# Kernel optimization log

Measured on AMD Instinct MI355X. Metric: run time of the kernel, lower is better.

## Reference

```python
import jax, jax.numpy as jnp
import numpy as np
import math

B, T, D_MODEL, N_HEADS = 4, 2048, 1024, 16
HEAD_DIM = D_MODEL // N_HEADS


def setup_inputs() -> dict:
    key = jax.random.key(0)
    k1, k2, k3 = jax.random.split(key, 3)
    x = jax.random.normal(k1, (B, T, D_MODEL), dtype=jnp.float32)
    # torch Linear weight layout: [out_features, in_features]
    w_qkv = jax.random.normal(k2, (3 * D_MODEL, D_MODEL), dtype=jnp.float32) * (1.0 / math.sqrt(D_MODEL))
    w_out = jax.random.normal(k3, (D_MODEL, D_MODEL), dtype=jnp.float32) * (1.0 / math.sqrt(D_MODEL))
    return {"x": x, "w_qkv": w_qkv, "w_out": w_out}


def reference(x, w_qkv, w_out):
    b, t, c = x.shape
    h, d = N_HEADS, HEAD_DIM
    # qkv projection: (B,T,3C) -> (3,B,H,T,D)
    qkv = jnp.einsum('btc,fc->btf', x, w_qkv)
    qkv = qkv.reshape(b, t, 3, h, d).transpose(2, 0, 3, 1, 4)
    q, k, v = qkv[0], qkv[1], qkv[2]
    scale = 1.0 / math.sqrt(d)
    # full O(T^2) attention scores, causal masked
    scores = jnp.einsum('bhqd,bhkd->bhqk', q, k) * scale
    causal = jnp.tril(jnp.ones((t, t), dtype=bool))
    scores = jnp.where(causal[None, None, :, :], scores, jnp.float32(-jnp.inf))
    attn = jax.nn.softmax(scores, axis=-1)
    out = jnp.einsum('bhqk,bhkd->bhqd', attn, v)  # (B,H,T,D)
    out = out.transpose(0, 2, 1, 3).reshape(b, t, c)
    out = jnp.einsum('btc,oc->bto', out, w_out)
    return out
```

## Files before the change

### kernel.cpp

```cpp
#include <hip/hip_runtime.h>
#include <hip/hip_bf16.h>

#define T_SEQ 2048
#define BATCH 4
#define NH    16
#define DM    1024
#define HD    64

typedef __attribute__((ext_vector_type(4))) float  f32x4;
typedef __attribute__((ext_vector_type(8))) short  s16x8;
typedef __attribute__((ext_vector_type(4))) short  s16x4;

__device__ __forceinline__ unsigned short f2b(float f) {
  union { float f; unsigned u; } v; v.f = f;
  unsigned u = v.u;
  unsigned r = 0x7fffu + ((u >> 16) & 1u);
  u += r;
  return (unsigned short)(u >> 16);
}

__device__ __forceinline__ f32x4 mfma16(s16x8 a, s16x8 b, f32x4 c) {
  return __builtin_amdgcn_mfma_f32_16x16x32_bf16(a, b, c, 0, 0, 0);
}

__device__ __forceinline__ float exp2_fast(float x) {
  float r; asm("v_exp_f32 %0, %1" : "=v"(r) : "v"(x)); return r;
}

__device__ __forceinline__ unsigned cvt_pk_bf16(float lo, float hi) {
  unsigned r; asm("v_cvt_pk_bf16_f32 %0, %1, %2" : "=v"(r) : "v"(lo), "v"(hi)); return r;
}

#define BAR() __builtin_amdgcn_s_barrier()
#define SCB() __builtin_amdgcn_sched_barrier(0)
#define LGK(n) do { asm volatile("s_waitcnt lgkmcnt(" #n ")" ::: "memory"); SCB(); } while (0)
#define VMC(n) do { asm volatile("s_waitcnt vmcnt(" #n ")" ::: "memory"); } while (0)

__global__ void cvt_all(const float* __restrict__ x, const float* __restrict__ wq,
                        const float* __restrict__ wo,
                        unsigned short* __restrict__ xb, unsigned short* __restrict__ wqb,
                        unsigned short* __restrict__ wob) {
  const int N4X = (BATCH * T_SEQ * DM) / 4;
  const int N4Q = (3 * DM * DM) / 4;
  const int N4O = (DM * DM) / 4;
  const int N4QSCALED = (DM * DM) / 4;
  int i = blockIdx.x * blockDim.x + threadIdx.x;
  int stride = gridDim.x * blockDim.x;
  for (int j = i; j < N4X + N4Q + N4O; j += stride) {
    const float* src; unsigned short* dst; int k; float scale = 1.f;
    if (j < N4X) { src = x; dst = xb; k = j; }
    else if (j < N4X + N4Q) {
      k = j - N4X; src = wq; dst = wqb;
      if (k < N4QSCALED) scale = 0.18033688011112042f;
    } else { k = j - N4X - N4Q; src = wo; dst = wob; }
    f32x4 v = ((const f32x4*)src)[k];
    s16x4 o;
    o.x = (short)f2b(v.x * scale); o.y = (short)f2b(v.y * scale);
    o.z = (short)f2b(v.z * scale); o.w = (short)f2b(v.w * scale);
    ((s16x4*)dst)[k] = o;
  }
}

__device__ __forceinline__ void rd4(s16x8 (&d)[4], const char* base, int rbase, int cb) {
#pragma unroll
  for (int j = 0; j < 4; ++j)
    d[j] = *(const s16x8*)(base + (rbase + j * 16) * 128 + cb);
}

__device__ __forceinline__ void stage_half(const unsigned short* __restrict__ Msrc,
                                           int rt0, int kt, char* lbase, int half,
                                           int srow8, int c2src, int c2lin, int Kd) {
#pragma unroll
  for (int q = 0; q < 2; ++q) {
    int rl = half * 128 + q * 64 + srow8;
    const char* src = (const char*)(Msrc + (size_t)(rt0 + rl) * Kd + kt) + c2src;
    __builtin_amdgcn_global_load_lds((const void*)src, (void*)(lbase + rl * 128 + c2lin),
                                     16, 0, 0);
  }
}

__device__ __forceinline__ void clust(f32x4 (&acc)[8][4], const s16x8 (&a)[4],
                                      const s16x8 (&b)[4], int mb) {
  __builtin_amdgcn_s_setprio(1);
#pragma unroll
  for (int j = 0; j < 4; ++j)
#pragma unroll
    for (int n = 0; n < 4; ++n)
      acc[mb + j][n] = mfma16(a[j], b[n], acc[mb + j][n]);
  __builtin_amdgcn_s_setprio(0);
}

__global__ __launch_bounds__(512, 2)
void gemm8p(const unsigned short* __restrict__ A, const unsigned short* __restrict__ B,
            unsigned short* __restrict__ C, int M, int N, int K) {
  __shared__ char smem[131072];
  char* A0b = smem;
  char* A1b = smem + 32768;
  char* B0b = smem + 65536;
  char* B1b = smem + 98304;

  const int tid = threadIdx.x;
  const int lane = tid & 63;
  const int w = tid >> 6;
  const int wm = w >> 2, wn = w & 3;
  const int lr = lane & 15, g = lane >> 4;

  const int gx = gridDim.x, nwg = gx * gridDim.y;
  const int bid = blockIdx.y * gx + blockIdx.x;
  const int cpx = nwg >> 3;
  const int b2 = (bid & 7) * cpx + (bid >> 3);
  const int row0 = (b2 % gx) * 256;
  const int col0 = (b2 / gx) * 256;

  const int srow8 = tid >> 3;
  const int c2lin = (tid & 7) * 16;
  const int c2src = ((tid & 7) ^ (srow8 & 7)) * 16;

  const int swz = (lr & 7) << 4;
  const int cs0 = (g * 16) ^ swz;
  const int cs1 = (64 + g * 16) ^ swz;
  const int rAlo = wm * 128 + lr;
  const int rAhi = rAlo + 64;
  const int rB = wn * 64 + lr;

  f32x4 acc[8][4] = {};
  s16x8 aP[4], aQ[4], aR[4], bP[4], bQ[4];

  const int NT = K / 64;

  stage_half(A, row0, 0, A0b, 0, srow8, c2src, c2lin, K);
  stage_half(A, row0, 0, A0b, 1, srow8, c2src, c2lin, K);
  stage_half(B, col0, 0, B0b, 0, srow8, c2src, c2lin, K);
  stage_half(B, col0, 0, B0b, 1, srow8, c2src, c2lin, K);
  stage_half(A, row0, 64, A1b, 0, srow8, c2src, c2lin, K);
  VMC(2);
  BAR();
  rd4(aP, A0b, rAlo, cs0);
  rd4(bP, B0b, rB, cs0);

  auto body = [&](char* Ac, char* Bc, char* An, char* Bn, int t) {
    const int ktn  = min(t + 1, NT - 1) * 64;
    const int ktn2 = min(t + 2, NT - 1) * 64;
    rd4(aQ, Ac, rAhi, cs0);
    stage_half(A, row0, ktn, An, 1, srow8, c2src, c2lin, K);
    BAR(); LGK(4);
    clust(acc, aP, bP, 0);
    BAR();
    rd4(aP, Ac, rAlo, cs1);
    rd4(aR, Ac, rAhi, cs1);
    rd4(bQ, Bc, rB, cs1);
    stage_half(B, col0, ktn, Bn, 0, srow8, c2src, c2lin, K);
    BAR(); LGK(12);
    clust(acc, aQ, bP, 4);
    BAR();
    stage_half(B, col0, ktn, Bn, 1, srow8, c2src, c2lin, K);
    BAR(); LGK(0);
    clust(acc, aP, bQ, 0);
    BAR();
    stage_half(A, row0, ktn2, Ac, 0, srow8, c2src, c2lin, K);
    VMC(2);
    BAR();
    rd4(aP, An, rAlo, cs0);
    rd4(bP, Bn, rB, cs0);
    clust(acc, aR, bQ, 4);
    BAR();
  };

#pragma unroll 1
  for (int tt = 0; tt < NT; tt += 2) {
    body(A0b, B0b, A1b, B1b, tt);
    body(A1b, B1b, A0b, B0b, tt + 1);
  }

#pragma unroll
  for (int m = 0; m < 8; ++m)
#pragma unroll
    for (int n = 0; n < 4; ++n)
#pragma unroll
      for (int i = 0; i < 4; ++i) {
        int row = row0 + wm * 128 + m * 16 + g * 4 + i;
        int col = col0 + wn * 64 + n * 16 + lr;
        C[(size_t)row * N + col] = f2b(acc[m][n][i]);
      }
}

template<int OUT_F32>
__global__ __launch_bounds__(256)
void gemm_bt(const unsigned short* __restrict__ A,
             const unsigned short* __restrict__ B,
             void* __restrict__ C, int M, int N, int K) {
  __shared__ unsigned short As[128 * 32];
  __shared__ unsigned short Bs[128 * 32];
  const int tid  = threadIdx.x;
  const int lane = tid & 63;
  const int w    = tid >> 6;
  const int wr   = w >> 1, wc = w & 1;
  const int lr   = lane & 15, g = lane >> 4;

  const int gx  = gridDim.x, nwg = gx * gridDim.y;
  const int bid = blockIdx.y * gx + blockIdx.x;
  const int cpx = nwg >> 3;
  const int b2  = (bid & 7) * cpx + (bid >> 3);
  const int row0 = (b2 % gx) * 128;
  const int col0 = (b2 / gx) * 128;

  const int srow = w * 16 + (lane >> 2);
  const int scol = (lane & 3) * 8;

  f32x4 acc[4][4] = {};

  for (int kt = 0; kt < K; kt += 32) {
    __syncthreads();
#pragma unroll
    for (int s = 0; s < 2; ++s) {
      const unsigned short* srcA = A + (size_t)(row0 + s * 64 + srow) * K + kt + scol;
      __builtin_amdgcn_global_load_lds((const void*)srcA, (void*)&As[(s * 64 + w * 16) * 32], 16, 0, 0);
      const unsigned short* srcB = B + (size_t)(col0 + s * 64 + srow) * K + kt + scol;
      __builtin_amdgcn_global_load_lds((const void*)srcB, (void*)&Bs[(s * 64 + w * 16) * 32], 16, 0, 0);
    }
    __syncthreads();

    s16x8 af[4], bf[4];
#pragma unroll
    for (int m = 0; m < 4; ++m)
      af[m] = *(const s16x8*)&As[(wr * 64 + m * 16 + lr) * 32 + g * 8];
#pragma unroll
    for (int n = 0; n < 4; ++n)
      bf[n] = *(const s16x8*)&Bs[(wc * 64 + n * 16 + lr) * 32 + g * 8];
#pragma unroll
    for (int m = 0; m < 4; ++m)
#pragma unroll
      for (int n = 0; n < 4; ++n)
        acc[m][n] = mfma16(af[m], bf[n], acc[m][n]);
  }

#pragma unroll
  for (int m = 0; m < 4; ++m)
#pragma unroll
    for (int n = 0; n < 4; ++n)
#pragma unroll
      for (int i = 0; i < 4; ++i) {
        int row = row0 + wr * 64 + m * 16 + g * 4 + i;
        int col = col0 + wc * 64 + n * 16 + lr;
        if (OUT_F32)
          ((float*)C)[(size_t)row * N + col] = acc[m][n][i];
        else
          ((unsigned short*)C)[(size_t)row * N + col] = f2b(acc[m][n][i]);
      }
}

__global__ __launch_bounds__(512)
void attn_kernel(const unsigned short* __restrict__ qkv,
                 unsigned short* __restrict__ out) {
  __shared__ unsigned short Ks[2][64 * 64];
  __shared__ unsigned short Vt[2][64 * 72];
  __shared__ unsigned short Ps[8][16 * 72];

  const int tid  = threadIdx.x;
  const int lane = tid & 63;
  const int w    = tid >> 6;
  const int lr   = lane & 15, g = lane >> 4;
  const int bid  = blockIdx.x;
  const int bh   = bid & 63;
  const int pi   = bid >> 6;
  const int b    = bh >> 4, h = bh & 15;
  const size_t rb = (size_t)b * T_SEQ;

  const bool grpV = (tid < 256);
  const int vd0 = (tid & 7) * 8, vr0 = (tid >> 3) * 2;
  const int t2  = tid - 256;
  const int kr0 = t2 >> 3, kc0 = t2 & 7;

#pragma unroll 1
  for (int ph = 0; ph < 2; ++ph) {
    const int qt = ph ? (15 - pi) : pi;
    const int q0 = qt * 128;
    const int qr = q0 + w * 16;
    const int qq = qr + lr;
    const int nt = 2 * qt + 2;
    const int qmax = qr + 15;

    s16x8 qf[2];
    {
      const unsigned short* qp = qkv + (rb + qq) * 3072 + h * 64;
      qf[0] = *(const s16x8*)(qp + g * 8);
      qf[1] = *(const s16x8*)(qp + 32 + g * 8);
    }

    float mI = -1e30f, lI = 0.f;
    f32x4 o[4] = {};

    s16x8 pre0, pre1;
    {
      if (grpV) {
        const unsigned short* vp = &qkv[(rb + vr0) * 3072 + 2048 + h * 64 + vd0];
        pre0 = *(const s16x8*)vp;
        pre1 = *(const s16x8*)(vp + 3072);
      } else {
        const unsigned short* kp = &qkv[(rb + kr0) * 3072 + 1024 + h * 64 + kc0 * 8];
        pre0 = *(const s16x8*)kp;
        pre1 = *(const s16x8*)(kp + 32 * 3072);
      }
    }

    for (int t = 0; t < nt; ++t) {
      const int cur = t & 1;
      if (grpV) {
#pragma unroll
        for (int jj = 0; jj < 8; ++jj) {
          int d = vd0 + jj;
          int sw = ((d ^ (d >> 3)) & 7) << 4;
          unsigned val = (unsigned)(unsigned short)pre0[jj] |
                         ((unsigned)(unsigned short)pre1[jj] << 16);
          *(unsigned*)((char*)&Vt[cur][0] + d * 144 + ((vr0 * 2) ^ sw)) = val;
        }
      } else {
        *(s16x8*)((char*)&Ks[cur][0] + kr0 * 128 + ((kc0 * 16) ^ ((kr0 & 7) << 4))) = pre0;
        int kr1 = kr0 + 32;
        *(s16x8*)((char*)&Ks[cur][0] + kr1 * 128 + ((kc0 * 16) ^ ((kr1 & 7) << 4))) = pre1;
      }
      __syncthreads();

      if (t + 1 < nt) {
        const int kv0n = (t + 1) * 64;
        if (grpV) {
          const unsigned short* vp = &qkv[(rb + kv0n + vr0) * 3072 + 2048 + h * 64 + vd0];
          pre0 = *(const s16x8*)vp;
          pre1 = *(const s16x8*)(vp + 3072);
        } else {
          const unsigned short* kp = &qkv[(rb + kv0n + kr0) * 3072 + 1024 + h * 64 + kc0 * 8];
          pre0 = *(const s16x8*)kp;
          pre1 = *(const s16x8*)(kp + 32 * 3072);
        }
      }

      const int kv0 = t * 64;
      if (kv0 <= qmax) {
        f32x4 s4[4];
        __builtin_amdgcn_s_setprio(1);
#pragma unroll
        for (int kc = 0; kc < 4; ++kc) {
          int row = kc * 16 + lr;
          const char* kbase = (const char*)&Ks[cur][0] + row * 128;
          int sw = (row & 7) << 4;
          s16x8 kf0 = *(const s16x8*)(kbase + ((g * 16) ^ sw));
          s16x8 kf1 = *(const s16x8*)(kbase + ((64 + g * 16) ^ sw));
          f32x4 s = {};
          s = mfma16(kf0, qf[0], s);
          s = mfma16(kf1, qf[1], s);
          s4[kc] = s;
        }
        __builtin_amdgcn_s_setprio(0);

        if (kv0 + 63 > qr) {
#pragma unroll
          for (int kc = 0; kc < 4; ++kc)
#pragma unroll
            for (int i = 0; i < 4; ++i) {
              int key = kv0 + kc * 16 + g * 4 + i;
              if (key > qq) s4[kc][i] = -1e30f;
            }
        }

        float mx = fmaxf(fmaxf(fmaxf(s4[0][0], s4[0][1]), fmaxf(s4[0][2], s4[0][3])),
                   fmaxf(fmaxf(fmaxf(s4[1][0], s4[1][1]), fmaxf(s4[1][2], s4[1][3])),
                   fmaxf(fmaxf(fmaxf(s4[2][0], s4[2][1]), fmaxf(s4[2][2], s4[2][3])),
                         fmaxf(fmaxf(s4[3][0], s4[3][1]), fmaxf(s4[3][2], s4[3][3])))));
        mx = fmaxf(mx, __shfl_xor(mx, 16));
        mx = fmaxf(mx, __shfl_xor(mx, 32));

        const bool defer = __all(mx - mI <= 11.5f);
        float alpha;
        if (defer) {
          alpha = 1.f;
        } else {
          float mn = fmaxf(mI, mx);
          alpha = exp2_fast(mI - mn);
          mI = mn;
        }
        float rs = 0.f;
#pragma unroll
        for (int kc = 0; kc < 4; ++kc)
#pragma unroll
          for (int i = 0; i < 4; ++i) {
            float p = exp2_fast(s4[kc][i] - mI);
            s4[kc][i] = p;
            rs += p;
          }
        rs += __shfl_xor(rs, 16);
        rs += __shfl_xor(rs, 32);
        lI = lI * alpha + rs;

        {
          char* pw = (char*)&Ps[w][0] + lr * 144;
#pragma unroll
          for (int kc = 0; kc < 4; ++kc) {
            unsigned v0 = cvt_pk_bf16(s4[kc][0], s4[kc][1]);
            unsigned v1 = cvt_pk_bf16(s4[kc][2], s4[kc][3]);
            unsigned long long pv = (unsigned long long)v0 | ((unsigned long long)v1 << 32);
            *(unsigned long long*)(pw + kc * 32 + g * 8) = pv;
          }
        }

        if (!defer) {
#pragma unroll
          for (int n = 0; n < 4; ++n)
#pragma unroll
            for (int i = 0; i < 4; ++i)
              o[n][i] *= alpha;
        }

        asm volatile("s_waitcnt lgkmcnt(0)" ::: "memory");

        __builtin_amdgcn_s_setprio(1);
#pragma unroll
        for (int kk = 0; kk < 2; ++kk) {
          s16x8 pf = *(const s16x8*)((const char*)&Ps[w][0] + lr * 144 + kk * 64 + g * 16);
#pragma unroll
          for (int n = 0; n < 4; ++n) {
            int d = n * 16 + lr;
            int sw = ((d ^ (d >> 3)) & 7) << 4;
            s16x8 vf = *(const s16x8*)((const char*)&Vt[cur][0] + d * 144 + ((kk * 64 + g * 16) ^ sw));
            o[n] = mfma16(vf, pf, o[n]);
          }
        }
        __builtin_amdgcn_s_setprio(0);
      }
    }

    float rl = 1.f / lI;
#pragma unroll
    for (int n = 0; n < 4; ++n) {
      unsigned p0 = cvt_pk_bf16(o[n][0] * rl, o[n][1] * rl);
      unsigned p1 = cvt_pk_bf16(o[n][2] * rl, o[n][3] * rl);
      unsigned long long pv = (unsigned long long)p0 | ((unsigned long long)p1 << 32);
      *(unsigned long long*)&out[(rb + qq) * 1024 + h * 64 + n * 16 + g * 4] = pv;
    }
  }
}

extern "C" void kernel_launch(void* const* d_in, const int* in_sizes, int n_in,
                              void* d_out, int out_size, void* d_ws, size_t ws_size,
                              hipStream_t stream) {
  const float* x     = (const float*)d_in[0];
  const float* w_qkv = (const float*)d_in[1];
  const float* w_out = (const float*)d_in[2];

  const size_t n_x   = (size_t)BATCH * T_SEQ * DM;
  const size_t n_wq  = (size_t)3 * DM * DM;
  const size_t n_wo  = (size_t)DM * DM;
  const size_t n_qkv = (size_t)BATCH * T_SEQ * 3 * DM;
  const size_t need  = (n_x + n_wq + n_wo + n_qkv + n_x) * 2;
  if (ws_size < need) return;

  unsigned short* xb  = (unsigned short*)d_ws;
  unsigned short* wqb = xb + n_x;
  unsigned short* wob = wqb + n_wq;
  unsigned short* qkv = wob + n_wo;
  unsigned short* att = qkv + n_qkv;

  cvt_all<<<2048, 256, 0, stream>>>(x, w_qkv, w_out, xb, wqb, wob);

  gemm8p<<<dim3(32, 12), 512, 0, stream>>>(xb, wqb, qkv, BATCH * T_SEQ, 3 * DM, DM);
  attn_kernel<<<512, 512, 0, stream>>>(qkv, att);
  gemm_bt<1><<<dim3(64, 8), 256, 0, stream>>>(att, wob, d_out, BATCH * T_SEQ, DM, DM);
}
```

Baseline: 190.2 us.

## Use 256x256 pipelined GEMM for output projection; fold max subtraction into MFMA init

The simple 128x128 output-projection GEMM is replaced by the templated 256x256 double-buffered gemm8p kernel, which gains an fp32 output mode. This cuts per-tile load overhead, but the grid shrinks to only 128 workgroups. In attention, the running max is now subtracted by seeding the QK^T MFMA accumulator with -mI, so scores come out already shifted. This removes the per-element subtraction in the common deferred-rescale path and moves the rescaling into the rare non-deferred branch.

```diff
diff --git a/kernel.cpp b/kernel.cpp
--- a/kernel.cpp
+++ b/kernel.cpp
@@ -90,9 +90,10 @@
   __builtin_amdgcn_s_setprio(0);
 }
 
+template<int OUTF32>
 __global__ __launch_bounds__(512, 2)
 void gemm8p(const unsigned short* __restrict__ A, const unsigned short* __restrict__ B,
-            unsigned short* __restrict__ C, int M, int N, int K) {
+            void* __restrict__ C, int M, int N, int K) {
   __shared__ char smem[131072];
   char* A0b = smem;
   char* A1b = smem + 32768;
@@ -180,69 +181,7 @@
       for (int i = 0; i < 4; ++i) {
         int row = row0 + wm * 128 + m * 16 + g * 4 + i;
         int col = col0 + wn * 64 + n * 16 + lr;
-        C[(size_t)row * N + col] = f2b(acc[m][n][i]);
-      }
-}
-
-template<int OUT_F32>
-__global__ __launch_bounds__(256)
-void gemm_bt(const unsigned short* __restrict__ A,
-             const unsigned short* __restrict__ B,
-             void* __restrict__ C, int M, int N, int K) {
-  __shared__ unsigned short As[128 * 32];
-  __shared__ unsigned short Bs[128 * 32];
-  const int tid  = threadIdx.x;
-  const int lane = tid & 63;
-  const int w    = tid >> 6;
-  const int wr   = w >> 1, wc = w & 1;
-  const int lr   = lane & 15, g = lane >> 4;
-
-  const int gx  = gridDim.x, nwg = gx * gridDim.y;
-  const int bid = blockIdx.y * gx + blockIdx.x;
-  const int cpx = nwg >> 3;
-  const int b2  = (bid & 7) * cpx + (bid >> 3);
-  const int row0 = (b2 % gx) * 128;
-  const int col0 = (b2 / gx) * 128;
-
-  const int srow = w * 16 + (lane >> 2);
-  const int scol = (lane & 3) * 8;
-
-  f32x4 acc[4][4] = {};
-
-  for (int kt = 0; kt < K; kt += 32) {
-    __syncthreads();
-#pragma unroll
-    for (int s = 0; s < 2; ++s) {
-      const unsigned short* srcA = A + (size_t)(row0 + s * 64 + srow) * K + kt + scol;
-      __builtin_amdgcn_global_load_lds((const void*)srcA, (void*)&As[(s * 64 + w * 16) * 32], 16, 0, 0);
-      const unsigned short* srcB = B + (size_t)(col0 + s * 64 + srow) * K + kt + scol;
-      __builtin_amdgcn_global_load_lds((const void*)srcB, (void*)&Bs[(s * 64 + w * 16) * 32], 16, 0, 0);
-    }
-    __syncthreads();
-
-    s16x8 af[4], bf[4];
-#pragma unroll
-    for (int m = 0; m < 4; ++m)
-      af[m] = *(const s16x8*)&As[(wr * 64 + m * 16 + lr) * 32 + g * 8];
-#pragma unroll
-    for (int n = 0; n < 4; ++n)
-      bf[n] = *(const s16x8*)&Bs[(wc * 64 + n * 16 + lr) * 32 + g * 8];
-#pragma unroll
-    for (int m = 0; m < 4; ++m)
-#pragma unroll
-      for (int n = 0; n < 4; ++n)
-        acc[m][n] = mfma16(af[m], bf[n], acc[m][n]);
-  }
-
-#pragma unroll
-  for (int m = 0; m < 4; ++m)
-#pragma unroll
-    for (int n = 0; n < 4; ++n)
-#pragma unroll
-      for (int i = 0; i < 4; ++i) {
-        int row = row0 + wr * 64 + m * 16 + g * 4 + i;
-        int col = col0 + wc * 64 + n * 16 + lr;
-        if (OUT_F32)
+        if (OUTF32)
           ((float*)C)[(size_t)row * N + col] = acc[m][n][i];
         else
           ((unsigned short*)C)[(size_t)row * N + col] = f2b(acc[m][n][i]);
@@ -287,7 +226,7 @@
       qf[1] = *(const s16x8*)(qp + 32 + g * 8);
     }
 
-    float mI = -1e30f, lI = 0.f;
+    float mI = 0.f, lI = 0.f;
     f32x4 o[4] = {};
 
     s16x8 pre0, pre1;
@@ -337,6 +276,8 @@
       const int kv0 = t * 64;
       if (kv0 <= qmax) {
         f32x4 s4[4];
+        f32x4 cini;
+        cini[0] = cini[1] = cini[2] = cini[3] = -mI;
         __builtin_amdgcn_s_setprio(1);
 #pragma unroll
         for (int kc = 0; kc < 4; ++kc) {
@@ -345,8 +286,7 @@
           int sw = (row & 7) << 4;
           s16x8 kf0 = *(const s16x8*)(kbase + ((g * 16) ^ sw));
           s16x8 kf1 = *(const s16x8*)(kbase + ((64 + g * 16) ^ sw));
-          f32x4 s = {};
-          s = mfma16(kf0, qf[0], s);
+          f32x4 s = mfma16(kf0, qf[0], cini);
           s = mfma16(kf1, qf[1], s);
           s4[kc] = s;
         }
@@ -362,34 +302,48 @@
             }
         }
 
-        float mx = fmaxf(fmaxf(fmaxf(s4[0][0], s4[0][1]), fmaxf(s4[0][2], s4[0][3])),
-                   fmaxf(fmaxf(fmaxf(s4[1][0], s4[1][1]), fmaxf(s4[1][2], s4[1][3])),
-                   fmaxf(fmaxf(fmaxf(s4[2][0], s4[2][1]), fmaxf(s4[2][2], s4[2][3])),
-                         fmaxf(fmaxf(s4[3][0], s4[3][1]), fmaxf(s4[3][2], s4[3][3])))));
+        float m0 = fmaxf(fmaxf(s4[0][0], s4[0][1]), s4[0][2]);
+        float m1 = fmaxf(fmaxf(s4[0][3], s4[1][0]), s4[1][1]);
+        float m2 = fmaxf(fmaxf(s4[1][2], s4[1][3]), s4[2][0]);
+        float m3 = fmaxf(fmaxf(s4[2][1], s4[2][2]), s4[2][3]);
+        float m4 = fmaxf(fmaxf(s4[3][0], s4[3][1]), s4[3][2]);
+        float mx = fmaxf(fmaxf(fmaxf(m0, m1), m2), fmaxf(fmaxf(m3, m4), s4[3][3]));
         mx = fmaxf(mx, __shfl_xor(mx, 16));
         mx = fmaxf(mx, __shfl_xor(mx, 32));
 
-        const bool defer = __all(mx - mI <= 11.5f);
-        float alpha;
+        const bool defer = __all(mx <= 11.5f);
+        float rs = 0.f;
         if (defer) {
-          alpha = 1.f;
+#pragma unroll
+          for (int kc = 0; kc < 4; ++kc)
+#pragma unroll
+            for (int i = 0; i < 4; ++i) {
+              float p = exp2_fast(s4[kc][i]);
+              s4[kc][i] = p;
+              rs += p;
+            }
         } else {
-          float mn = fmaxf(mI, mx);
-          alpha = exp2_fast(mI - mn);
-          mI = mn;
-        }
-        float rs = 0.f;
-#pragma unroll
-        for (int kc = 0; kc < 4; ++kc)
-#pragma unroll
-          for (int i = 0; i < 4; ++i) {
-            float p = exp2_fast(s4[kc][i] - mI);
-            s4[kc][i] = p;
-            rs += p;
-          }
+          float mxp = fmaxf(mx, 0.f);
+          mI += mxp;
+          float al = exp2_fast(-mxp);
+#pragma unroll
+          for (int kc = 0; kc < 4; ++kc)
+#pragma unroll
+            for (int i = 0; i < 4; ++i) {
+              float p = exp2_fast(s4[kc][i] - mxp);
+              s4[kc][i] = p;
+              rs += p;
+            }
+#pragma unroll
+          for (int n = 0; n < 4; ++n)
+#pragma unroll
+            for (int i = 0; i < 4; ++i)
+              o[n][i] *= al;
+          lI *= al;
+        }
         rs += __shfl_xor(rs, 16);
         rs += __shfl_xor(rs, 32);
-        lI = lI * alpha + rs;
+        lI += rs;
 
         {
           char* pw = (char*)&Ps[w][0] + lr * 144;
@@ -400,14 +354,6 @@
             unsigned long long pv = (unsigned long long)v0 | ((unsigned long long)v1 << 32);
             *(unsigned long long*)(pw + kc * 32 + g * 8) = pv;
           }
-        }
-
-        if (!defer) {
-#pragma unroll
-          for (int n = 0; n < 4; ++n)
-#pragma unroll
-            for (int i = 0; i < 4; ++i)
-              o[n][i] *= alpha;
         }
 
         asm volatile("s_waitcnt lgkmcnt(0)" ::: "memory");
@@ -461,7 +407,7 @@
 
   cvt_all<<<2048, 256, 0, stream>>>(x, w_qkv, w_out, xb, wqb, wob);
 
-  gemm8p<<<dim3(32, 12), 512, 0, stream>>>(xb, wqb, qkv, BATCH * T_SEQ, 3 * DM, DM);
+  gemm8p<0><<<dim3(32, 12), 512, 0, stream>>>(xb, wqb, qkv, BATCH * T_SEQ, 3 * DM, DM);
   attn_kernel<<<512, 512, 0, stream>>>(qkv, att);
-  gemm_bt<1><<<dim3(64, 8), 256, 0, stream>>>(att, wob, d_out, BATCH * T_SEQ, DM, DM);
-}
+  gemm8p<1><<<dim3(32, 4), 512, 0, stream>>>(att, wob, d_out, BATCH * T_SEQ, DM, DM);
+}
```

Result: slower. 208.5 us (+9.6%).
